# Performance work log

Measured on AMD Instinct MI355X. Metric: run time of the kernel, lower is better.

The kernel has to match this reference:

```python
import jax, jax.numpy as jnp
import numpy as np

N = 16384          # nodes/edges
F = 128            # features per rank
L_MAX = 3
SIZES = [1, 3, 9, 27]   # 3^l components for l = 0..3

def _doublefactorial(n):
    x = 1
    for i in range(1, n + 1, 2):
        x *= i
    return x

def _factorial(n):
    x = 1
    for i in range(1, n + 1):
        x *= i
    return x

def _norm_l1l2l3(l1, l2, l3):
    # even-parity recoupling normalization (verbatim from source)
    J = l1 + l2 + l3
    J1 = J - 2 * l1 - 1
    J2 = J - 2 * l2 - 1
    J3 = J - 2 * l3 - 1
    num = (_factorial(l1) * _factorial(l2) * _doublefactorial(2 * l3 - 1)
           * _factorial((J1 + 1) // 2) * _factorial((J2 + 1) // 2))
    den = (_factorial(l3) * _doublefactorial(J1) * _doublefactorial(J2)
           * _doublefactorial(J3) * _factorial(J // 2))
    return num / den

# All even-parity recoupling paths (l1, l2, l3): triangle inequality + even l1+l2-l3.
PATHS = [(l1, l2, l3)
         for l3 in range(L_MAX + 1)
         for l1 in range(L_MAX + 1)
         for l2 in range(L_MAX + 1)
         if abs(l1 - l2) <= l3 <= l1 + l2 and (l1 + l2 - l3) % 2 == 0]
N_PATHS = len(PATHS)  # == 23 == _get_n_paths(3,3,3)

def setup_inputs() -> dict:
    key = jax.random.key(0)
    k1, k2, k3 = jax.random.split(key, 3)
    x = jax.random.normal(k1, (N, F * sum(SIZES)), dtype=jnp.float32)
    y = jax.random.normal(k2, (N, F * sum(SIZES)), dtype=jnp.float32)
    weights = jax.random.normal(k3, (N_PATHS, F), dtype=jnp.float32)
    return {"x": x, "y": y, "weights": weights}

def _split(t):
    # flat [N, F*40] -> list of [N, F, 3,...,3] (rank-l Cartesian blocks)
    blocks, off = [], 0
    for l, s in enumerate(SIZES):
        blocks.append(t[:, off:off + F * s].reshape((-1, F) + (3,) * l))
        off += F * s
    return blocks

def reference(x, y, weights):
    xs = _split(x)
    ys = _split(y)
    outs = [jnp.zeros((x.shape[0], F) + (3,) * l3, x.dtype) for l3 in range(L_MAX + 1)]
    for p, (l1, l2, l3) in enumerate(PATHS):
        k = (l1 + l2 - l3) // 2          # number of contracted Cartesian indices
        xa = 'abc'[:l1 - k]              # free indices from x
        c = 'uvw'[:k]                    # contracted indices
        yb = 'deg'[:l2 - k]              # free indices from y
        sub = f"nf{xa}{c},nf{c}{yb}->nf{xa}{yb}"
        z = jnp.einsum(sub, xs[l1], ys[l2])           # [N, F, 3^l3]
        w = weights[p].reshape((1, F) + (1,) * l3)    # per-path per-feature weight
        outs[l3] = outs[l3] + jnp.asarray(_norm_l1l2l3(l1, l2, l3), x.dtype) * w * z
    return jnp.concatenate([o.reshape(o.shape[0], -1) for o in outs], axis=1)
```

## Files before the change

### kernel.cpp

```cpp
#include <hip/hip_runtime.h>


#define FF 128
#define ROW 5120
#define HALFROW 2560

typedef float floatx4 __attribute__((ext_vector_type(4)));

__device__ __constant__ float NORMS[23] = {
    1.0f, 1.0f, 2.0f/3.0f, 0.4f,
    1.0f, 1.0f, 1.0f, 1.0f, 2.0f/3.0f, 2.0f/3.0f,
    1.0f, 0.75f, 1.0f, 1.0f, 1.0f, 1.0f, 0.75f,
    1.0f, 5.0f/9.0f, 5.0f/9.0f, 5.0f/6.0f, 1.0f, 5.0f/6.0f
};

#define GL2LDS(g, l)  __builtin_amdgcn_global_load_lds(                      \
        (const __attribute__((address_space(1))) void*)(g),                  \
        (__attribute__((address_space(3))) void*)(l), 16, 0, 0)

__global__ __launch_bounds__(128, 2) void wtp_kernel(
    const float* __restrict__ x, const float* __restrict__ y,
    const float* __restrict__ w, float* __restrict__ out, int n_nodes)
{
    __shared__ float buf[2][2 * HALFROW];

    const int tid   = threadIdx.x;
    const int f     = tid & 63;
    const int half  = tid >> 6;
    const int wbase = half * 256;

    const int bslot = blockIdx.x & 511;
    const int fbase = (blockIdx.x >> 9) << 6;
    const int chunk = n_nodes >> 9;
    const int first = bslot * chunk;

    int goff[5];
    #pragma unroll
    for (int i = 0; i < 5; ++i) {
        const int o = i * 512 + tid * 4;
        int r;
        if      (o < 64)  r = fbase        + o;
        else if (o < 256) r = 128 + fbase*3  + (o - 64);
        else if (o < 832) r = 512 + fbase*9  + (o - 256);
        else              r = 1664 + fbase*27 + (o - 832);
        goff[i] = r;
    }

    {
        const float* xr = x + (size_t)first * ROW;
        const float* yr = y + (size_t)first * ROW;
        #pragma unroll
        for (int i = 0; i < 5; ++i) {
            GL2LDS(xr + goff[i], &buf[0][i * 512 + wbase]);
            GL2LDS(yr + goff[i], &buf[0][HALFROW + i * 512 + wbase]);
        }
    }

    float c[23];
    #pragma unroll
    for (int p = 0; p < 23; ++p) c[p] = NORMS[p] * w[p * FF + fbase + f];

    int cur = 0;
    for (int k = 0; k < chunk; ++k) {
        const int node = first + k;

        if (k + 1 < chunk) {
            const float* xr = x + (size_t)(node + 1) * ROW;
            const float* yr = y + (size_t)(node + 1) * ROW;
            float* nb = &buf[cur ^ 1][0];
            #pragma unroll
            for (int i = 0; i < 5; ++i) {
                GL2LDS(xr + goff[i], nb + i * 512 + wbase);
                GL2LDS(yr + goff[i], nb + HALFROW + i * 512 + wbase);
            }
            if (k == 0) {
                asm volatile("s_waitcnt vmcnt(10)" ::: "memory");
            } else {
                asm volatile("s_waitcnt vmcnt(15)" ::: "memory");
            }
        } else {
            asm volatile("s_waitcnt vmcnt(0)" ::: "memory");
        }
        __builtin_amdgcn_s_barrier();

        const float* bx = &buf[cur][0];
        const float* by = &buf[cur][HALFROW];
        const float x0 = bx[f], y0 = by[f];
        float x1[3], y1[3], x2[9], y2[9];
        #pragma unroll
        for (int j = 0; j < 3; ++j)  x1[j] = bx[64  + f*3 + j];
        #pragma unroll
        for (int j = 0; j < 3; ++j)  y1[j] = by[64  + f*3 + j];
        #pragma unroll
        for (int j = 0; j < 9; ++j)  x2[j] = bx[256 + f*9 + j];
        #pragma unroll
        for (int j = 0; j < 9; ++j)  y2[j] = by[256 + f*9 + j];

        const float* bx3 = bx + 832 + f*27;
        const float* by3 = by + 832 + f*27;

        float o0, o1[3], o2[9], o3[27];

        if (half == 0) {
            {
                float acc = c[0] * (x0 * y0);
                float d3 = 0.f;
                #pragma unroll
                for (int u = 0; u < 3; ++u) d3 += x1[u] * y1[u];
                acc += c[1] * d3;
                float d9 = 0.f;
                #pragma unroll
                for (int t = 0; t < 9; ++t) d9 += x2[t] * y2[t];
                acc += c[2] * d9;
                float d27 = 0.f;
                #pragma unroll
                for (int t = 0; t < 27; ++t) d27 += bx3[t] * by3[t];
                acc += c[3] * d27;
                o0 = acc;
            }
            #pragma unroll
            for (int d = 0; d < 3; ++d) {
                float acc = c[4] * (x0 * y1[d]) + c[5] * (x1[d] * y0);
                float s6 = 0.f, s7 = 0.f, s8 = 0.f, s9 = 0.f;
                #pragma unroll
                for (int u = 0; u < 3; ++u) s6 += x1[u] * y2[u*3 + d];
                #pragma unroll
                for (int u = 0; u < 3; ++u) s7 += x2[d*3 + u] * y1[u];
                #pragma unroll
                for (int t = 0; t < 9; ++t) s8 += x2[t] * by3[t*3 + d];
                #pragma unroll
                for (int t = 0; t < 9; ++t) s9 += bx3[d*9 + t] * y2[t];
                o1[d] = acc + c[6]*s6 + c[7]*s7 + c[8]*s8 + c[9]*s9;
            }
            #pragma unroll
            for (int t = 0; t < 9; ++t) {
                const int a = t / 3, d = t % 3;
                float acc = c[10] * (x0 * y2[t]) + c[11] * (x1[a] * y1[d])
                          + c[13] * (x2[t] * y0);
                float s12 = 0.f, s14 = 0.f, s15 = 0.f, s16 = 0.f;
                #pragma unroll
                for (int u = 0; u < 3; ++u) s12 += x1[u] * by3[u*9 + t];
                #pragma unroll
                for (int u = 0; u < 3; ++u) s14 += x2[a*3 + u] * y2[u*3 + d];
                #pragma unroll
                for (int u = 0; u < 3; ++u) s15 += bx3[t*3 + u] * y1[u];
                #pragma unroll
                for (int s = 0; s < 9; ++s) s16 += bx3[a*9 + s] * by3[s*3 + d];
                o2[t] = acc + c[12]*s12 + c[14]*s14 + c[15]*s15 + c[16]*s16;
            }
        } else {
            #pragma unroll
            for (int q = 0; q < 27; ++q) {
                const int a = q / 9, t9 = q % 9, r = q / 3, e = q % 3;
                float acc = c[17] * (x0 * by3[q]) + c[18] * (x1[a] * y2[t9])
                          + c[19] * (x2[r] * y1[e]) + c[21] * (bx3[q] * y0);
                float s20 = 0.f, s22 = 0.f;
                #pragma unroll
                for (int u = 0; u < 3; ++u) s20 += x2[a*3 + u] * by3[u*9 + t9];
                #pragma unroll
                for (int u = 0; u < 3; ++u) s22 += bx3[r*3 + u] * y2[u*3 + e];
                o3[q] = acc + c[20]*s20 + c[22]*s22;
            }
        }

        asm volatile("s_waitcnt lgkmcnt(0)" ::: "memory");
        __builtin_amdgcn_s_barrier();

        float* B = &buf[cur][0];
        if (half == 0) {
            B[f] = o0;
            #pragma unroll
            for (int d = 0; d < 3; ++d) B[64  + f*3 + d] = o1[d];
            #pragma unroll
            for (int t = 0; t < 9; ++t) B[256 + f*9 + t] = o2[t];
        } else {
            #pragma unroll
            for (int q = 0; q < 27; ++q) B[832 + f*27 + q] = o3[q];
        }
        asm volatile("s_waitcnt lgkmcnt(0)" ::: "memory");
        __builtin_amdgcn_s_barrier();

        float* orow = out + (size_t)node * ROW;
        #pragma unroll
        for (int i = 0; i < 5; ++i) {
            floatx4 v = *(const floatx4*)(B + i * 512 + tid * 4);
            __builtin_nontemporal_store(v, (floatx4*)(orow + goff[i]));
        }
        asm volatile("s_waitcnt lgkmcnt(0)" ::: "memory");
        __builtin_amdgcn_s_barrier();
        cur ^= 1;
    }
}

extern "C" void kernel_launch(void* const* d_in, const int* in_sizes, int n_in,
                              void* d_out, int out_size, void* d_ws, size_t ws_size,
                              hipStream_t stream) {
    const float* x = (const float*)d_in[0];
    const float* y = (const float*)d_in[1];
    const float* w = (const float*)d_in[2];
    float* out = (float*)d_out;

    const int n_nodes = in_sizes[0] / ROW;
    dim3 grid(1024), block(128);
    hipLaunchKernelGGL(wtp_kernel, grid, block, 0, stream, x, y, w, out, n_nodes);
}
```

Measured before the change: 217.7 us.

## Replace persistent per-block node loop with one block per node pair

The persistent grid of 1024 blocks, each looping over a contiguous chunk of nodes with double-buffered LDS prefetch, is replaced by a grid of n_nodes blocks. Each block handles exactly two nodes for one 64-feature half, issuing both nodes' loads up front and computing them in turn. This spreads the work over many more blocks to expose more memory-level parallelism and drop the loop and pipelining control. In exchange, every block reloads its 23 weights and the steady-state prefetch overlap inside a block is lost. The launch-bounds occupancy hint is also relaxed.

```diff
diff --git a/kernel.cpp b/kernel.cpp
--- a/kernel.cpp
+++ b/kernel.cpp
@@ -18,177 +18,185 @@
         (const __attribute__((address_space(1))) void*)(g),                  \
         (__attribute__((address_space(3))) void*)(l), 16, 0, 0)
 
-__global__ __launch_bounds__(128, 2) void wtp_kernel(
+__device__ __forceinline__ void compute_node(
+    const float* __restrict__ bx, const float* __restrict__ by,
+    const float* __restrict__ c, int f, int h,
+    float& o0, float* o1, float* o2, float* o3)
+{
+    const float x0 = bx[f], y0 = by[f];
+    float x1[3], y1[3], x2[9], y2[9];
+    #pragma unroll
+    for (int j = 0; j < 3; ++j)  x1[j] = bx[64  + f*3 + j];
+    #pragma unroll
+    for (int j = 0; j < 3; ++j)  y1[j] = by[64  + f*3 + j];
+    #pragma unroll
+    for (int j = 0; j < 9; ++j)  x2[j] = bx[256 + f*9 + j];
+    #pragma unroll
+    for (int j = 0; j < 9; ++j)  y2[j] = by[256 + f*9 + j];
+
+    const float* bx3 = bx + 832 + f*27;
+    const float* by3 = by + 832 + f*27;
+
+    if (h == 0) {
+        {
+            float acc = c[0] * (x0 * y0);
+            float d3 = 0.f;
+            #pragma unroll
+            for (int u = 0; u < 3; ++u) d3 += x1[u] * y1[u];
+            acc += c[1] * d3;
+            float d9 = 0.f;
+            #pragma unroll
+            for (int t = 0; t < 9; ++t) d9 += x2[t] * y2[t];
+            acc += c[2] * d9;
+            float d27 = 0.f;
+            #pragma unroll
+            for (int t = 0; t < 27; ++t) d27 += bx3[t] * by3[t];
+            acc += c[3] * d27;
+            o0 = acc;
+        }
+        #pragma unroll
+        for (int d = 0; d < 3; ++d) {
+            float acc = c[4] * (x0 * y1[d]) + c[5] * (x1[d] * y0);
+            float s6 = 0.f, s7 = 0.f, s8 = 0.f, s9 = 0.f;
+            #pragma unroll
+            for (int u = 0; u < 3; ++u) s6 += x1[u] * y2[u*3 + d];
+            #pragma unroll
+            for (int u = 0; u < 3; ++u) s7 += x2[d*3 + u] * y1[u];
+            #pragma unroll
+            for (int t = 0; t < 9; ++t) s8 += x2[t] * by3[t*3 + d];
+            #pragma unroll
+            for (int t = 0; t < 9; ++t) s9 += bx3[d*9 + t] * y2[t];
+            o1[d] = acc + c[6]*s6 + c[7]*s7 + c[8]*s8 + c[9]*s9;
+        }
+        #pragma unroll
+        for (int t = 0; t < 9; ++t) {
+            const int a = t / 3, d = t % 3;
+            float acc = c[10] * (x0 * y2[t]) + c[11] * (x1[a] * y1[d])
+                      + c[13] * (x2[t] * y0);
+            float s12 = 0.f, s14 = 0.f, s15 = 0.f, s16 = 0.f;
+            #pragma unroll
+            for (int u = 0; u < 3; ++u) s12 += x1[u] * by3[u*9 + t];
+            #pragma unroll
+            for (int u = 0; u < 3; ++u) s14 += x2[a*3 + u] * y2[u*3 + d];
+            #pragma unroll
+            for (int u = 0; u < 3; ++u) s15 += bx3[t*3 + u] * y1[u];
+            #pragma unroll
+            for (int s = 0; s < 9; ++s) s16 += bx3[a*9 + s] * by3[s*3 + d];
+            o2[t] = acc + c[12]*s12 + c[14]*s14 + c[15]*s15 + c[16]*s16;
+        }
+    } else {
+        #pragma unroll
+        for (int q = 0; q < 27; ++q) {
+            const int a = q / 9, t9 = q % 9, r = q / 3, e = q % 3;
+            float acc = c[17] * (x0 * by3[q]) + c[18] * (x1[a] * y2[t9])
+                      + c[19] * (x2[r] * y1[e]) + c[21] * (bx3[q] * y0);
+            float s20 = 0.f, s22 = 0.f;
+            #pragma unroll
+            for (int u = 0; u < 3; ++u) s20 += x2[a*3 + u] * by3[u*9 + t9];
+            #pragma unroll
+            for (int u = 0; u < 3; ++u) s22 += bx3[r*3 + u] * y2[u*3 + e];
+            o3[q] = acc + c[20]*s20 + c[22]*s22;
+        }
+    }
+}
+
+__device__ __forceinline__ void stage_outputs(
+    float* __restrict__ B, int f, int h,
+    float o0, const float* o1, const float* o2, const float* o3)
+{
+    if (h == 0) {
+        B[f] = o0;
+        #pragma unroll
+        for (int d = 0; d < 3; ++d) B[64  + f*3 + d] = o1[d];
+        #pragma unroll
+        for (int t = 0; t < 9; ++t) B[256 + f*9 + t] = o2[t];
+    } else {
+        #pragma unroll
+        for (int q = 0; q < 27; ++q) B[832 + f*27 + q] = o3[q];
+    }
+}
+
+__global__ __launch_bounds__(128) void wtp_kernel(
     const float* __restrict__ x, const float* __restrict__ y,
-    const float* __restrict__ w, float* __restrict__ out, int n_nodes)
+    const float* __restrict__ w, float* __restrict__ out)
 {
-    __shared__ float buf[2][2 * HALFROW];
+    __shared__ float bufA[2 * HALFROW];
+    __shared__ float bufB[2 * HALFROW];
 
     const int tid   = threadIdx.x;
     const int f     = tid & 63;
     const int half  = tid >> 6;
     const int wbase = half * 256;
 
-    const int bslot = blockIdx.x & 511;
-    const int fbase = (blockIdx.x >> 9) << 6;
-    const int chunk = n_nodes >> 9;
-    const int first = bslot * chunk;
+    const int n0    = (blockIdx.x >> 1) * 2;
+    const int fbase = (blockIdx.x & 1) << 6;
+
+    const float* xA = x + (size_t)n0 * ROW;
+    const float* yA = y + (size_t)n0 * ROW;
+    const float* xB = xA + ROW;
+    const float* yB = yA + ROW;
+    float* orowA    = out + (size_t)n0 * ROW;
+    float* orowB    = orowA + ROW;
 
     int goff[5];
     #pragma unroll
     for (int i = 0; i < 5; ++i) {
         const int o = i * 512 + tid * 4;
         int r;
-        if      (o < 64)  r = fbase        + o;
-        else if (o < 256) r = 128 + fbase*3  + (o - 64);
-        else if (o < 832) r = 512 + fbase*9  + (o - 256);
+        if      (o < 64)  r = fbase          + o;
+        else if (o < 256) r = 128  + fbase*3  + (o - 64);
+        else if (o < 832) r = 512  + fbase*9  + (o - 256);
         else              r = 1664 + fbase*27 + (o - 832);
         goff[i] = r;
     }
 
-    {
-        const float* xr = x + (size_t)first * ROW;
-        const float* yr = y + (size_t)first * ROW;
-        #pragma unroll
-        for (int i = 0; i < 5; ++i) {
-            GL2LDS(xr + goff[i], &buf[0][i * 512 + wbase]);
-            GL2LDS(yr + goff[i], &buf[0][HALFROW + i * 512 + wbase]);
-        }
-    }
-
+    #pragma unroll
+    for (int i = 0; i < 5; ++i) {
+        GL2LDS(xA + goff[i], bufA + i * 512 + wbase);
+        GL2LDS(yA + goff[i], bufA + HALFROW + i * 512 + wbase);
+    }
     float c[23];
     #pragma unroll
     for (int p = 0; p < 23; ++p) c[p] = NORMS[p] * w[p * FF + fbase + f];
-
-    int cur = 0;
-    for (int k = 0; k < chunk; ++k) {
-        const int node = first + k;
-
-        if (k + 1 < chunk) {
-            const float* xr = x + (size_t)(node + 1) * ROW;
-            const float* yr = y + (size_t)(node + 1) * ROW;
-            float* nb = &buf[cur ^ 1][0];
-            #pragma unroll
-            for (int i = 0; i < 5; ++i) {
-                GL2LDS(xr + goff[i], nb + i * 512 + wbase);
-                GL2LDS(yr + goff[i], nb + HALFROW + i * 512 + wbase);
-            }
-            if (k == 0) {
-                asm volatile("s_waitcnt vmcnt(10)" ::: "memory");
-            } else {
-                asm volatile("s_waitcnt vmcnt(15)" ::: "memory");
-            }
-        } else {
-            asm volatile("s_waitcnt vmcnt(0)" ::: "memory");
-        }
-        __builtin_amdgcn_s_barrier();
-
-        const float* bx = &buf[cur][0];
-        const float* by = &buf[cur][HALFROW];
-        const float x0 = bx[f], y0 = by[f];
-        float x1[3], y1[3], x2[9], y2[9];
-        #pragma unroll
-        for (int j = 0; j < 3; ++j)  x1[j] = bx[64  + f*3 + j];
-        #pragma unroll
-        for (int j = 0; j < 3; ++j)  y1[j] = by[64  + f*3 + j];
-        #pragma unroll
-        for (int j = 0; j < 9; ++j)  x2[j] = bx[256 + f*9 + j];
-        #pragma unroll
-        for (int j = 0; j < 9; ++j)  y2[j] = by[256 + f*9 + j];
-
-        const float* bx3 = bx + 832 + f*27;
-        const float* by3 = by + 832 + f*27;
-
-        float o0, o1[3], o2[9], o3[27];
-
-        if (half == 0) {
-            {
-                float acc = c[0] * (x0 * y0);
-                float d3 = 0.f;
-                #pragma unroll
-                for (int u = 0; u < 3; ++u) d3 += x1[u] * y1[u];
-                acc += c[1] * d3;
-                float d9 = 0.f;
-                #pragma unroll
-                for (int t = 0; t < 9; ++t) d9 += x2[t] * y2[t];
-                acc += c[2] * d9;
-                float d27 = 0.f;
-                #pragma unroll
-                for (int t = 0; t < 27; ++t) d27 += bx3[t] * by3[t];
-                acc += c[3] * d27;
-                o0 = acc;
-            }
-            #pragma unroll
-            for (int d = 0; d < 3; ++d) {
-                float acc = c[4] * (x0 * y1[d]) + c[5] * (x1[d] * y0);
-                float s6 = 0.f, s7 = 0.f, s8 = 0.f, s9 = 0.f;
-                #pragma unroll
-                for (int u = 0; u < 3; ++u) s6 += x1[u] * y2[u*3 + d];
-                #pragma unroll
-                for (int u = 0; u < 3; ++u) s7 += x2[d*3 + u] * y1[u];
-                #pragma unroll
-                for (int t = 0; t < 9; ++t) s8 += x2[t] * by3[t*3 + d];
-                #pragma unroll
-                for (int t = 0; t < 9; ++t) s9 += bx3[d*9 + t] * y2[t];
-                o1[d] = acc + c[6]*s6 + c[7]*s7 + c[8]*s8 + c[9]*s9;
-            }
-            #pragma unroll
-            for (int t = 0; t < 9; ++t) {
-                const int a = t / 3, d = t % 3;
-                float acc = c[10] * (x0 * y2[t]) + c[11] * (x1[a] * y1[d])
-                          + c[13] * (x2[t] * y0);
-                float s12 = 0.f, s14 = 0.f, s15 = 0.f, s16 = 0.f;
-                #pragma unroll
-                for (int u = 0; u < 3; ++u) s12 += x1[u] * by3[u*9 + t];
-                #pragma unroll
-                for (int u = 0; u < 3; ++u) s14 += x2[a*3 + u] * y2[u*3 + d];
-                #pragma unroll
-                for (int u = 0; u < 3; ++u) s15 += bx3[t*3 + u] * y1[u];
-                #pragma unroll
-                for (int s = 0; s < 9; ++s) s16 += bx3[a*9 + s] * by3[s*3 + d];
-                o2[t] = acc + c[12]*s12 + c[14]*s14 + c[15]*s15 + c[16]*s16;
-            }
-        } else {
-            #pragma unroll
-            for (int q = 0; q < 27; ++q) {
-                const int a = q / 9, t9 = q % 9, r = q / 3, e = q % 3;
-                float acc = c[17] * (x0 * by3[q]) + c[18] * (x1[a] * y2[t9])
-                          + c[19] * (x2[r] * y1[e]) + c[21] * (bx3[q] * y0);
-                float s20 = 0.f, s22 = 0.f;
-                #pragma unroll
-                for (int u = 0; u < 3; ++u) s20 += x2[a*3 + u] * by3[u*9 + t9];
-                #pragma unroll
-                for (int u = 0; u < 3; ++u) s22 += bx3[r*3 + u] * y2[u*3 + e];
-                o3[q] = acc + c[20]*s20 + c[22]*s22;
-            }
-        }
-
-        asm volatile("s_waitcnt lgkmcnt(0)" ::: "memory");
-        __builtin_amdgcn_s_barrier();
-
-        float* B = &buf[cur][0];
-        if (half == 0) {
-            B[f] = o0;
-            #pragma unroll
-            for (int d = 0; d < 3; ++d) B[64  + f*3 + d] = o1[d];
-            #pragma unroll
-            for (int t = 0; t < 9; ++t) B[256 + f*9 + t] = o2[t];
-        } else {
-            #pragma unroll
-            for (int q = 0; q < 27; ++q) B[832 + f*27 + q] = o3[q];
-        }
-        asm volatile("s_waitcnt lgkmcnt(0)" ::: "memory");
-        __builtin_amdgcn_s_barrier();
-
-        float* orow = out + (size_t)node * ROW;
-        #pragma unroll
-        for (int i = 0; i < 5; ++i) {
-            floatx4 v = *(const floatx4*)(B + i * 512 + tid * 4);
-            __builtin_nontemporal_store(v, (floatx4*)(orow + goff[i]));
-        }
-        asm volatile("s_waitcnt lgkmcnt(0)" ::: "memory");
-        __builtin_amdgcn_s_barrier();
-        cur ^= 1;
+    #pragma unroll
+    for (int i = 0; i < 5; ++i) {
+        GL2LDS(xB + goff[i], bufB + i * 512 + wbase);
+        GL2LDS(yB + goff[i], bufB + HALFROW + i * 512 + wbase);
+    }
+
+    asm volatile("s_waitcnt vmcnt(10)" ::: "memory");
+    __builtin_amdgcn_s_barrier();
+
+    float o0, o1[3], o2[9], o3[27];
+    compute_node(bufA, bufA + HALFROW, c, f, half, o0, o1, o2, o3);
+
+    asm volatile("s_waitcnt lgkmcnt(0)" ::: "memory");
+    __builtin_amdgcn_s_barrier();
+    stage_outputs(bufA, f, half, o0, o1, o2, o3);
+    asm volatile("s_waitcnt lgkmcnt(0)" ::: "memory");
+    __builtin_amdgcn_s_barrier();
+
+    #pragma unroll
+    for (int i = 0; i < 5; ++i) {
+        floatx4 v = *(const floatx4*)(bufA + i * 512 + tid * 4);
+        __builtin_nontemporal_store(v, (floatx4*)(orowA + goff[i]));
+    }
+
+    asm volatile("s_waitcnt vmcnt(5)" ::: "memory");
+    __builtin_amdgcn_s_barrier();
+
+    compute_node(bufB, bufB + HALFROW, c, f, half, o0, o1, o2, o3);
+
+    asm volatile("s_waitcnt lgkmcnt(0)" ::: "memory");
+    __builtin_amdgcn_s_barrier();
+    stage_outputs(bufB, f, half, o0, o1, o2, o3);
+    asm volatile("s_waitcnt lgkmcnt(0)" ::: "memory");
+    __builtin_amdgcn_s_barrier();
+
+    #pragma unroll
+    for (int i = 0; i < 5; ++i) {
+        floatx4 v = *(const floatx4*)(bufB + i * 512 + tid * 4);
+        __builtin_nontemporal_store(v, (floatx4*)(orowB + goff[i]));
     }
 }
 
@@ -201,6 +209,6 @@
     float* out = (float*)d_out;
 
     const int n_nodes = in_sizes[0] / ROW;
-    dim3 grid(1024), block(128);
-    hipLaunchKernelGGL(wtp_kernel, grid, block, 0, stream, x, y, w, out, n_nodes);
-}
+    dim3 grid(n_nodes), block(128);
+    hipLaunchKernelGGL(wtp_kernel, grid, block, 0, stream, x, y, w, out);
+}
```

Result: faster. 181.7 us (-16.5%).
